# Kernel optimization log

Hardware: AMD Instinct MI355X
Metric: run time of the kernel (lower is better)

Reference implementation:

```python
import jax, jax.numpy as jnp
import numpy as np

B, LX, LY, D = 8, 2048, 2048, 256

def setup_inputs() -> dict:
    key = jax.random.key(0)
    k1, k2, k3, k4 = jax.random.split(key, 4)
    x = jax.random.normal(k1, (B, LX, D), dtype=jnp.float32)
    y = jax.random.normal(k2, (B, LY, D), dtype=jnp.float32)
    y_mask = jax.random.randint(k3, (B, LY), 0, 2).astype(jnp.bool_)
    W = jax.random.normal(k4, (D, D), dtype=jnp.float32) * (1.0 / np.sqrt(D))
    b = jnp.zeros((D,), dtype=jnp.float32)
    return {"x": x, "y": y, "y_mask": y_mask, "W": W, "b": b}

def reference(x, y, y_mask, W, b):
    # shared linear + relu projection (torch Linear: x @ W.T + b)
    x_proj = jax.nn.relu(jnp.einsum('bld,ed->ble', x, W) + b)  # [B,LX,D]
    y_proj = jax.nn.relu(jnp.einsum('bld,ed->ble', y, W) + b)  # [B,LY,D]
    scores = jnp.einsum('bxd,byd->bxy', x_proj, y_proj)        # [B,LX,LY]
    scores = jnp.where(y_mask[:, None, :], -jnp.inf, scores)
    alpha = jax.nn.softmax(scores, axis=-1)                    # [B,LX,LY]
    return jnp.einsum('bxy,byd->bxd', alpha, y)                # [B,LX,D]
```

## Files before the change

### kernel.cpp

```cpp
#include <hip/hip_runtime.h>

typedef __attribute__((ext_vector_type(8))) short short8;
typedef _Float16 half8 __attribute__((ext_vector_type(8)));
typedef __attribute__((ext_vector_type(4))) float f32x4;
typedef __attribute__((ext_vector_type(4))) unsigned int uint4v;
typedef __attribute__((ext_vector_type(2))) unsigned int uint2v;

#define B_   8
#define LX_  2048
#define LY_  2048
#define D_   256
#define NROW (B_ * LX_)
#define NQ   4

__device__ __forceinline__ unsigned short f2bf(float f) {
  unsigned u = __builtin_bit_cast(unsigned, f);
  u += 0x7FFF + ((u >> 16) & 1);
  return (unsigned short)(u >> 16);
}
__device__ __forceinline__ float bf2f(unsigned short h) {
  unsigned u = ((unsigned)h) << 16;
  return __builtin_bit_cast(float, u);
}

__global__ __launch_bounds__(256) void prep_kernel(
    const float* __restrict__ W, unsigned short* __restrict__ Whi,
    unsigned short* __restrict__ Wlo,
    const int* __restrict__ MASK, int* __restrict__ CIDX,
    int* __restrict__ CPOS, int* __restrict__ Lc) {
  int t = threadIdx.x;
  if (blockIdx.x >= 8) {
    int base = (blockIdx.x - 8) * 2048 + t * 8;
    f32x4 f0 = *(const f32x4*)(W + base);
    f32x4 f1 = *(const f32x4*)(W + base + 4);
    float v[8] = {f0[0], f0[1], f0[2], f0[3], f1[0], f1[1], f1[2], f1[3]};
    unsigned short h[8], l[8];
    for (int j = 0; j < 8; ++j) {
      h[j] = f2bf(v[j]);
      l[j] = f2bf(v[j] - bf2f(h[j]));
    }
    uint4v vh = {(unsigned)h[0] | ((unsigned)h[1] << 16), (unsigned)h[2] | ((unsigned)h[3] << 16),
                 (unsigned)h[4] | ((unsigned)h[5] << 16), (unsigned)h[6] | ((unsigned)h[7] << 16)};
    uint4v vl = {(unsigned)l[0] | ((unsigned)l[1] << 16), (unsigned)l[2] | ((unsigned)l[3] << 16),
                 (unsigned)l[4] | ((unsigned)l[5] << 16), (unsigned)l[6] | ((unsigned)l[7] << 16)};
    *(uint4v*)(Whi + base) = vh;
    *(uint4v*)(Wlo + base) = vl;
    return;
  }
  __shared__ int s[256];
  int b = blockIdx.x;
  int f[8];
  int cnt = 0;
  for (int k = 0; k < 8; ++k) {
    f[k] = (MASK[b * 2048 + t * 8 + k] == 0) ? 1 : 0;
    cnt += f[k];
  }
  s[t] = cnt;
  __syncthreads();
  for (int off = 1; off < 256; off <<= 1) {
    int v = (t >= off) ? s[t - off] : 0;
    __syncthreads();
    s[t] += v;
    __syncthreads();
  }
  if (t == 255) Lc[b] = s[255];
  int off = s[t] - cnt;
  for (int k = 0; k < 8; ++k) {
    int j = t * 8 + k;
    if (f[k]) {
      CIDX[b * 2048 + off] = j;
      CPOS[b * 2048 + j] = b * 2048 + off;
      ++off;
    } else {
      CPOS[b * 2048 + j] = -1;
    }
  }
}

__global__ __launch_bounds__(256, 2) void projgather_kernel(
    const float* __restrict__ X, const float* __restrict__ Y,
    const float* __restrict__ bias,
    const unsigned short* __restrict__ Whi, const unsigned short* __restrict__ Wlo,
    const int* __restrict__ CPOS, const int* __restrict__ CIDX,
    const int* __restrict__ Lc,
    _Float16* __restrict__ XP, _Float16* __restrict__ YPc,
    _Float16* __restrict__ YTc) {
  __shared__ __align__(16) unsigned char smem[51200];
  int t = threadIdx.x;

  if (blockIdx.x >= 512) {
    _Float16 (*tile)[72] = (_Float16(*)[72])smem;
    int id = blockIdx.x - 512;
    int db = id & 3, nb = (id >> 2) & 31, b = id >> 7;
    int lc = Lc[b];
    int end = (lc + 31) & ~31;
    if (nb * 64 >= end) return;
    int nl = t >> 2, ds = t & 3;
    int j = nb * 64 + nl;
    int idx = (j < lc) ? CIDX[b * 2048 + j] : 0;
    const float* src = Y + (size_t)(b * LY_ + idx) * D_ + db * 64 + ds * 16;
    for (int i = 0; i < 4; ++i) {
      f32x4 f = *(const f32x4*)(src + i * 4);
      for (int k = 0; k < 4; ++k) tile[ds * 16 + i * 4 + k][nl] = (_Float16)f[k];
    }
    __syncthreads();
    int dl = t >> 2, nsub = t & 3;
    uint4v v0 = *(const uint4v*)&tile[dl][nsub * 16];
    uint4v v1 = *(const uint4v*)&tile[dl][nsub * 16 + 8];
    _Float16* dst = YTc + (size_t)(b * D_ + db * 64 + dl) * LY_ + nb * 64 + nsub * 16;
    *(uint4v*)(dst) = v0;
    *(uint4v*)(dst + 8) = v1;
    return;
  }

  unsigned short (*Ah)[40] = (unsigned short(*)[40])(smem);
  unsigned short (*Al)[40] = (unsigned short(*)[40])(smem + 5120);
  unsigned short (*Bh)[40] = (unsigned short(*)[40])(smem + 10240);
  unsigned short (*Bl)[40] = (unsigned short(*)[40])(smem + 30720);

  int lane = t & 63, wave = t >> 6;
  int q = lane >> 4, n15 = lane & 15;

  bool isX = blockIdx.x < 256;
  const float* src = isX ? X : Y;
  int m0 = (isX ? blockIdx.x : (blockIdx.x - 256)) * 64;

  f32x4 acc[4][4];
  for (int mt = 0; mt < 4; ++mt)
    for (int nt = 0; nt < 4; ++nt) acc[mt][nt] = (f32x4){0.f, 0.f, 0.f, 0.f};

  int arow = t >> 2, aseg = t & 3;
  int erow = t >> 2, ec = t & 3;

  f32x4 pa[2];
  uint4v pbh[4], pbl[4];
#define PROJ_PF(kc)                                                            \
  {                                                                            \
    for (int i = 0; i < 2; ++i)                                                \
      pa[i] = *(const f32x4*)(src + (size_t)(m0 + arow) * D_ + (kc) * 32 +     \
                              (aseg + i * 4) * 4);                             \
    for (int p = 0; p < 4; ++p) {                                              \
      int e = p * 64 + erow;                                                   \
      pbh[p] = *(const uint4v*)(Whi + (size_t)e * D_ + (kc) * 32 + ec * 8);    \
      pbl[p] = *(const uint4v*)(Wlo + (size_t)e * D_ + (kc) * 32 + ec * 8);    \
    }                                                                          \
  }

  PROJ_PF(0);

  for (int kc = 0; kc < 8; ++kc) {
    __syncthreads();
    for (int i = 0; i < 2; ++i) {
      int seg = aseg + i * 4;
      f32x4 f = pa[i];
      unsigned short h[4], l[4];
      for (int j = 0; j < 4; ++j) {
        h[j] = f2bf(f[j]);
        l[j] = f2bf(f[j] - bf2f(h[j]));
      }
      uint2v vh = {(unsigned)h[0] | ((unsigned)h[1] << 16),
                   (unsigned)h[2] | ((unsigned)h[3] << 16)};
      uint2v vl = {(unsigned)l[0] | ((unsigned)l[1] << 16),
                   (unsigned)l[2] | ((unsigned)l[3] << 16)};
      *(uint2v*)&Ah[arow][seg * 4] = vh;
      *(uint2v*)&Al[arow][seg * 4] = vl;
    }
    for (int p = 0; p < 4; ++p) {
      int e = p * 64 + erow;
      *(uint4v*)&Bh[e][ec * 8] = pbh[p];
      *(uint4v*)&Bl[e][ec * 8] = pbl[p];
    }
    if (kc < 7) PROJ_PF(kc + 1);
    __syncthreads();

    short8 afh[4], afl[4], bfh[4], bfl[4];
    for (int mt = 0; mt < 4; ++mt) {
      afh[mt] = *(const short8*)&Ah[mt * 16 + n15][q * 8];
      afl[mt] = *(const short8*)&Al[mt * 16 + n15][q * 8];
    }
    for (int nt = 0; nt < 4; ++nt) {
      bfh[nt] = *(const short8*)&Bh[wave * 64 + nt * 16 + n15][q * 8];
      bfl[nt] = *(const short8*)&Bl[wave * 64 + nt * 16 + n15][q * 8];
    }
    for (int mt = 0; mt < 4; ++mt)
      for (int nt = 0; nt < 4; ++nt) {
        acc[mt][nt] = __builtin_amdgcn_mfma_f32_16x16x32_bf16(afh[mt], bfh[nt], acc[mt][nt], 0, 0, 0);
        acc[mt][nt] = __builtin_amdgcn_mfma_f32_16x16x32_bf16(afl[mt], bfh[nt], acc[mt][nt], 0, 0, 0);
        acc[mt][nt] = __builtin_amdgcn_mfma_f32_16x16x32_bf16(afh[mt], bfl[nt], acc[mt][nt], 0, 0, 0);
      }
  }
#undef PROJ_PF

  int drow[16];
  for (int mt = 0; mt < 4; ++mt)
    for (int r = 0; r < 4; ++r) {
      int row = m0 + mt * 16 + q * 4 + r;
      drow[mt * 4 + r] = isX ? row : CPOS[row];
    }
  _Float16* dst = isX ? XP : YPc;
  for (int nt = 0; nt < 4; ++nt) {
    int e = wave * 64 + nt * 16 + n15;
    float bv = bias[e];
    for (int mt = 0; mt < 4; ++mt)
      for (int r = 0; r < 4; ++r) {
        int dr = drow[mt * 4 + r];
        if (dr >= 0) {
          float v = acc[mt][nt][r] + bv;
          v = v > 0.f ? v : 0.f;
          dst[(size_t)dr * D_ + e] = (_Float16)v;
        }
      }
  }
}

__global__ __launch_bounds__(256, 2) void flash_kernel(
    const _Float16* __restrict__ XP, const _Float16* __restrict__ YPc,
    const _Float16* __restrict__ YTc, const int* __restrict__ Lc,
    _Float16* __restrict__ PO, float* __restrict__ Pm, float* __restrict__ Pl) {
  __shared__ _Float16 yp_t[32][264];
  __shared__ _Float16 yT_t[256][40];
  __shared__ _Float16 pbuf[4][16][40];

  int t = threadIdx.x;
  int lane = t & 63, wave = t >> 6;
  int q = lane >> 4, n15 = lane & 15;
  int qtr = blockIdx.x & 3;
  int xb = (blockIdx.x >> 2) & 31;
  int b = blockIdx.x >> 7;
  int row0 = xb * 64 + wave * 16;

  int lc = Lc[b];
  int T = (lc + 31) >> 5;
  int tstart = (T * qtr) >> 2;
  int tend   = (T * (qtr + 1)) >> 2;

  half8 a[8];
  const _Float16* xrow = XP + (size_t)(b * LX_ + row0 + n15) * D_ + q * 8;
  for (int kk = 0; kk < 8; ++kk) a[kk] = *(const half8*)(xrow + kk * 32);

  half8 lones;
  for (int j = 0; j < 8; ++j) lones[j] = (n15 == 0) ? (_Float16)1 : (_Float16)0;

  float m_r[4];
  for (int r = 0; r < 4; ++r) m_r[r] = -1e30f;
  f32x4 lacc = {0.f, 0.f, 0.f, 0.f};
  f32x4 oacc[16];
  for (int dt = 0; dt < 16; ++dt) oacc[dt] = (f32x4){0.f, 0.f, 0.f, 0.f};

  const _Float16* ypb = YPc + (size_t)b * LY_ * D_;
  const _Float16* yTb = YTc + (size_t)b * D_ * LY_;

  uint4v pr[8];
#define PREFETCH(tt)                                                          \
  {                                                                           \
    int y0p = (tt) * 32;                                                      \
    for (int i = 0; i < 4; ++i) {                                             \
      int c = t + i * 256;                                                    \
      pr[i] = *(const uint4v*)(ypb + (size_t)(y0p + (c >> 5)) * D_ + (c & 31) * 8); \
    }                                                                         \
    for (int i = 0; i < 4; ++i) {                                             \
      int c = t + i * 256;                                                    \
      pr[4 + i] = *(const uint4v*)(yTb + (size_t)(c >> 2) * LY_ + y0p + (c & 3) * 8); \
    }                                                                         \
  }

  if (tstart < tend) PREFETCH(tstart);

  for (int tt = tstart; tt < tend; ++tt) {
    int y0 = tt * 32;
    __syncthreads();
    for (int i = 0; i < 4; ++i) {
      int c = t + i * 256;
      *(uint4v*)&yp_t[c >> 5][(c & 31) * 8] = pr[i];
    }
    for (int i = 0; i < 4; ++i) {
      int c = t + i * 256;
      *(uint4v*)&yT_t[c >> 2][(c & 3) * 8] = pr[4 + i];
    }
    if (tt + 1 < tend) PREFETCH(tt + 1);
    __syncthreads();

    f32x4 S0 = {0.f, 0.f, 0.f, 0.f}, S1 = {0.f, 0.f, 0.f, 0.f};
    for (int kk = 0; kk < 8; ++kk) {
      half8 b0 = *(const half8*)&yp_t[n15][kk * 32 + q * 8];
      S0 = __builtin_amdgcn_mfma_f32_16x16x32_f16(a[kk], b0, S0, 0, 0, 0);
    }
    for (int kk = 0; kk < 8; ++kk) {
      half8 b1 = *(const half8*)&yp_t[16 + n15][kk * 32 + q * 8];
      S1 = __builtin_amdgcn_mfma_f32_16x16x32_f16(a[kk], b1, S1, 0, 0, 0);
    }
    bool mk0 = (y0 + n15) >= lc;
    bool mk1 = (y0 + 16 + n15) >= lc;

    float al[4];
    _Float16 ph0[4], ph1[4];
    bool need = false;
    for (int r = 0; r < 4; ++r) {
      float s0 = mk0 ? -1e30f : S0[r];
      float s1 = mk1 ? -1e30f : S1[r];
      float tm = fmaxf(s0, s1);
      tm = fmaxf(tm, __shfl_xor(tm, 1));
      tm = fmaxf(tm, __shfl_xor(tm, 2));
      tm = fmaxf(tm, __shfl_xor(tm, 4));
      tm = fmaxf(tm, __shfl_xor(tm, 8));
      float mn = fmaxf(m_r[r], tm);
      al[r] = __expf(m_r[r] - mn);
      m_r[r] = mn;
      ph0[r] = (_Float16)__expf(s0 - mn);
      ph1[r] = (_Float16)__expf(s1 - mn);
      need = need || (al[r] != 1.0f);
    }
    if (__ballot(need)) {
      for (int dt = 0; dt < 16; ++dt)
        for (int r = 0; r < 4; ++r) oacc[dt][r] *= al[r];
      for (int r = 0; r < 4; ++r) lacc[r] *= al[r];
    }
    for (int r = 0; r < 4; ++r) {
      pbuf[wave][q * 4 + r][n15] = ph0[r];
      pbuf[wave][q * 4 + r][16 + n15] = ph1[r];
    }
    half8 pa = *(const half8*)&pbuf[wave][n15][q * 8];
    lacc = __builtin_amdgcn_mfma_f32_16x16x32_f16(pa, lones, lacc, 0, 0, 0);
    for (int dt = 0; dt < 16; ++dt) {
      half8 bb = *(const half8*)&yT_t[dt * 16 + n15][q * 8];
      oacc[dt] = __builtin_amdgcn_mfma_f32_16x16x32_f16(pa, bb, oacc[dt], 0, 0, 0);
    }
  }
#undef PREFETCH

  size_t prow = (size_t)(qtr * B_ + b) * LX_ + row0;
  _Float16* po = PO + prow * D_;
  for (int dt = 0; dt < 16; ++dt)
    for (int r = 0; r < 4; ++r)
      po[(size_t)(q * 4 + r) * D_ + dt * 16 + n15] = (_Float16)oacc[dt][r];
  if (n15 == 0) {
    for (int r = 0; r < 4; ++r) {
      Pm[prow + q * 4 + r] = m_r[r];
      Pl[prow + q * 4 + r] = lacc[r];
    }
  }
}

__global__ __launch_bounds__(256) void merge_kernel(
    const _Float16* __restrict__ PO, const float* __restrict__ Pm,
    const float* __restrict__ Pl, float* __restrict__ OUT) {
  int c = blockIdx.x * 256 + threadIdx.x;
  int row = c >> 5, seg = c & 31;
  float m = -1e30f;
  float mh[NQ], lh[NQ];
  for (int h = 0; h < NQ; ++h) {
    mh[h] = Pm[(size_t)h * NROW + row];
    lh[h] = Pl[(size_t)h * NROW + row];
    m = fmaxf(m, mh[h]);
  }
  float l = 0.f;
  float wh[NQ];
  for (int h = 0; h < NQ; ++h) {
    wh[h] = __expf(mh[h] - m);
    l += lh[h] * wh[h];
  }
  float inv = 1.0f / l;
  float o[8];
  for (int j = 0; j < 8; ++j) o[j] = 0.f;
  for (int h = 0; h < NQ; ++h) {
    half8 a = *(const half8*)(PO + ((size_t)h * NROW + row) * D_ + seg * 8);
    float w = wh[h];
    for (int j = 0; j < 8; ++j) o[j] += (float)a[j] * w;
  }
  float* op = OUT + (size_t)row * D_ + seg * 8;
  f32x4 o0 = {o[0] * inv, o[1] * inv, o[2] * inv, o[3] * inv};
  f32x4 o1 = {o[4] * inv, o[5] * inv, o[6] * inv, o[7] * inv};
  *(f32x4*)op = o0;
  *(f32x4*)(op + 4) = o1;
}

extern "C" void kernel_launch(void* const* d_in, const int* in_sizes, int n_in,
                              void* d_out, int out_size, void* d_ws, size_t ws_size,
                              hipStream_t stream) {
  const float* x     = (const float*)d_in[0];
  const float* y     = (const float*)d_in[1];
  const int*   ymask = (const int*)  d_in[2];
  const float* W     = (const float*)d_in[3];
  const float* bias  = (const float*)d_in[4];
  float* out = (float*)d_out;

  char* ws = (char*)d_ws;
  size_t o = 0;
  unsigned short* Whi = (unsigned short*)(ws + o); o += 131072;
  unsigned short* Wlo = (unsigned short*)(ws + o); o += 131072;
  _Float16* XP  = (_Float16*)(ws + o); o += 8388608;
  _Float16* YPc = (_Float16*)(ws + o); o += 8388608;
  _Float16* YTc = (_Float16*)(ws + o); o += 8388608;
  _Float16* PO  = (_Float16*)(ws + o); o += (size_t)NQ * NROW * D_ * 2;
  float* Pm   = (float*)(ws + o); o += (size_t)NQ * NROW * 4;
  float* Pl   = (float*)(ws + o); o += (size_t)NQ * NROW * 4;
  int*   CIDX = (int*)  (ws + o); o += 65536;
  int*   CPOS = (int*)  (ws + o); o += 65536;
  int*   Lc   = (int*)  (ws + o);

  prep_kernel<<<40, 256, 0, stream>>>(W, Whi, Wlo, ymask, CIDX, CPOS, Lc);
  projgather_kernel<<<1536, 256, 0, stream>>>(x, y, bias, Whi, Wlo, CPOS, CIDX, Lc,
                                              XP, YPc, YTc);
  flash_kernel<<<1024, 256, 0, stream>>>(XP, YPc, YTc, Lc, PO, Pm, Pl);
  merge_kernel<<<2048, 256, 0, stream>>>(PO, Pm, Pl, out);
}
```

Before: 165.5 us.

## Project only unmasked Y rows and halve flash split-KV partitions

The Y projection now gathers rows through the compacted index list and skips blocks past the unmasked count, so masked rows are never projected. The scattered CPOS writes are replaced by staging the tile in shared memory and writing whole rows with coalesced vector stores. The flash kernel splits the key range into two partitions instead of four, which halves the grid and the partial-output traffic and simplifies the merge. The risk is lower occupancy and less parallelism in the flash kernel, which now has 512 blocks.

```diff
diff --git a/kernel.cpp b/kernel.cpp
--- a/kernel.cpp
+++ b/kernel.cpp
@@ -11,7 +11,6 @@
 #define LY_  2048
 #define D_   256
 #define NROW (B_ * LX_)
-#define NQ   4
 
 __device__ __forceinline__ unsigned short f2bf(float f) {
   unsigned u = __builtin_bit_cast(unsigned, f);
@@ -26,8 +25,7 @@
 __global__ __launch_bounds__(256) void prep_kernel(
     const float* __restrict__ W, unsigned short* __restrict__ Whi,
     unsigned short* __restrict__ Wlo,
-    const int* __restrict__ MASK, int* __restrict__ CIDX,
-    int* __restrict__ CPOS, int* __restrict__ Lc) {
+    const int* __restrict__ MASK, int* __restrict__ CIDX, int* __restrict__ Lc) {
   int t = threadIdx.x;
   if (blockIdx.x >= 8) {
     int base = (blockIdx.x - 8) * 2048 + t * 8;
@@ -67,13 +65,7 @@
   int off = s[t] - cnt;
   for (int k = 0; k < 8; ++k) {
     int j = t * 8 + k;
-    if (f[k]) {
-      CIDX[b * 2048 + off] = j;
-      CPOS[b * 2048 + j] = b * 2048 + off;
-      ++off;
-    } else {
-      CPOS[b * 2048 + j] = -1;
-    }
+    if (f[k]) CIDX[b * 2048 + (off++)] = j;
   }
 }
 
@@ -81,8 +73,7 @@
     const float* __restrict__ X, const float* __restrict__ Y,
     const float* __restrict__ bias,
     const unsigned short* __restrict__ Whi, const unsigned short* __restrict__ Wlo,
-    const int* __restrict__ CPOS, const int* __restrict__ CIDX,
-    const int* __restrict__ Lc,
+    const int* __restrict__ CIDX, const int* __restrict__ Lc,
     _Float16* __restrict__ XP, _Float16* __restrict__ YPc,
     _Float16* __restrict__ YTc) {
   __shared__ __align__(16) unsigned char smem[51200];
@@ -120,25 +111,37 @@
 
   int lane = t & 63, wave = t >> 6;
   int q = lane >> 4, n15 = lane & 15;
+  int arow = t >> 2, aseg = t & 3;
+  int erow = t >> 2, ec = t & 3;
 
   bool isX = blockIdx.x < 256;
-  const float* src = isX ? X : Y;
-  int m0 = (isX ? blockIdx.x : (blockIdx.x - 256)) * 64;
+  int m0 = 0, b = 0, slot0 = 0, lcb = 0;
+  const float* arow_ptr;
+  if (isX) {
+    m0 = blockIdx.x * 64;
+    arow_ptr = X + (size_t)(m0 + arow) * D_;
+  } else {
+    int id = blockIdx.x - 256;
+    b = id >> 5;
+    int rb = id & 31;
+    lcb = Lc[b];
+    slot0 = rb * 64;
+    if (slot0 >= lcb) return;
+    int sl = slot0 + arow;
+    int grow = (sl < lcb) ? CIDX[b * 2048 + sl] : 0;
+    arow_ptr = Y + (size_t)(b * 2048 + grow) * D_;
+  }
 
   f32x4 acc[4][4];
   for (int mt = 0; mt < 4; ++mt)
     for (int nt = 0; nt < 4; ++nt) acc[mt][nt] = (f32x4){0.f, 0.f, 0.f, 0.f};
-
-  int arow = t >> 2, aseg = t & 3;
-  int erow = t >> 2, ec = t & 3;
 
   f32x4 pa[2];
   uint4v pbh[4], pbl[4];
 #define PROJ_PF(kc)                                                            \
   {                                                                            \
     for (int i = 0; i < 2; ++i)                                                \
-      pa[i] = *(const f32x4*)(src + (size_t)(m0 + arow) * D_ + (kc) * 32 +     \
-                              (aseg + i * 4) * 4);                             \
+      pa[i] = *(const f32x4*)(arow_ptr + (kc) * 32 + (aseg + i * 4) * 4);      \
     for (int p = 0; p < 4; ++p) {                                              \
       int e = p * 64 + erow;                                                   \
       pbh[p] = *(const uint4v*)(Whi + (size_t)e * D_ + (kc) * 32 + ec * 8);    \
@@ -191,25 +194,28 @@
   }
 #undef PROJ_PF
 
-  int drow[16];
-  for (int mt = 0; mt < 4; ++mt)
-    for (int r = 0; r < 4; ++r) {
-      int row = m0 + mt * 16 + q * 4 + r;
-      drow[mt * 4 + r] = isX ? row : CPOS[row];
-    }
-  _Float16* dst = isX ? XP : YPc;
+  __syncthreads();
+  _Float16 (*epi)[264] = (_Float16(*)[264])smem;
   for (int nt = 0; nt < 4; ++nt) {
     int e = wave * 64 + nt * 16 + n15;
     float bv = bias[e];
     for (int mt = 0; mt < 4; ++mt)
       for (int r = 0; r < 4; ++r) {
-        int dr = drow[mt * 4 + r];
-        if (dr >= 0) {
-          float v = acc[mt][nt][r] + bv;
-          v = v > 0.f ? v : 0.f;
-          dst[(size_t)dr * D_ + e] = (_Float16)v;
-        }
+        float v = acc[mt][nt][r] + bv;
+        v = v > 0.f ? v : 0.f;
+        epi[mt * 16 + q * 4 + r][e] = (_Float16)v;
       }
+  }
+  __syncthreads();
+  int row = t >> 2, seg = t & 3;
+  bool valid = isX || (slot0 + row < lcb);
+  if (valid) {
+    _Float16* drp = isX ? (XP + (size_t)(m0 + row) * D_)
+                        : (YPc + (size_t)(b * 2048 + slot0 + row) * D_);
+    for (int k = 0; k < 8; ++k) {
+      uint4v v = *(const uint4v*)&epi[row][seg * 64 + k * 8];
+      *(uint4v*)(drp + seg * 64 + k * 8) = v;
+    }
   }
 }
 
@@ -224,15 +230,16 @@
   int t = threadIdx.x;
   int lane = t & 63, wave = t >> 6;
   int q = lane >> 4, n15 = lane & 15;
-  int qtr = blockIdx.x & 3;
-  int xb = (blockIdx.x >> 2) & 31;
-  int b = blockIdx.x >> 7;
+  int half = blockIdx.x & 1;
+  int xb = (blockIdx.x >> 1) & 31;
+  int b = blockIdx.x >> 6;
   int row0 = xb * 64 + wave * 16;
 
   int lc = Lc[b];
-  int T = (lc + 31) >> 5;
-  int tstart = (T * qtr) >> 2;
-  int tend   = (T * (qtr + 1)) >> 2;
+  int T  = (lc + 31) >> 5;
+  int T0 = (T + 1) >> 1;
+  int tstart = half ? T0 : 0;
+  int tend   = half ? T  : T0;
 
   half8 a[8];
   const _Float16* xrow = XP + (size_t)(b * LX_ + row0 + n15) * D_ + q * 8;
@@ -328,7 +335,7 @@
   }
 #undef PREFETCH
 
-  size_t prow = (size_t)(qtr * B_ + b) * LX_ + row0;
+  size_t prow = (size_t)(half * B_ + b) * LX_ + row0;
   _Float16* po = PO + prow * D_;
   for (int dt = 0; dt < 16; ++dt)
     for (int r = 0; r < 4; ++r)
@@ -346,32 +353,21 @@
     const float* __restrict__ Pl, float* __restrict__ OUT) {
   int c = blockIdx.x * 256 + threadIdx.x;
   int row = c >> 5, seg = c & 31;
-  float m = -1e30f;
-  float mh[NQ], lh[NQ];
-  for (int h = 0; h < NQ; ++h) {
-    mh[h] = Pm[(size_t)h * NROW + row];
-    lh[h] = Pl[(size_t)h * NROW + row];
-    m = fmaxf(m, mh[h]);
-  }
-  float l = 0.f;
-  float wh[NQ];
-  for (int h = 0; h < NQ; ++h) {
-    wh[h] = __expf(mh[h] - m);
-    l += lh[h] * wh[h];
-  }
-  float inv = 1.0f / l;
-  float o[8];
-  for (int j = 0; j < 8; ++j) o[j] = 0.f;
-  for (int h = 0; h < NQ; ++h) {
-    half8 a = *(const half8*)(PO + ((size_t)h * NROW + row) * D_ + seg * 8);
-    float w = wh[h];
-    for (int j = 0; j < 8; ++j) o[j] += (float)a[j] * w;
-  }
-  float* op = OUT + (size_t)row * D_ + seg * 8;
-  f32x4 o0 = {o[0] * inv, o[1] * inv, o[2] * inv, o[3] * inv};
-  f32x4 o1 = {o[4] * inv, o[5] * inv, o[6] * inv, o[7] * inv};
-  *(f32x4*)op = o0;
-  *(f32x4*)(op + 4) = o1;
+  float m0 = Pm[row], m1 = Pm[NROW + row];
+  float l0 = Pl[row], l1 = Pl[NROW + row];
+  float m = fmaxf(m0, m1);
+  float w0 = __expf(m0 - m), w1 = __expf(m1 - m);
+  float inv = 1.0f / (l0 * w0 + l1 * w1);
+  const _Float16* p0 = PO + (size_t)row * D_ + seg * 8;
+  const _Float16* p1 = p0 + (size_t)NROW * D_;
+  half8 a = *(const half8*)p0;
+  half8 bsec = *(const half8*)p1;
+  float* o = OUT + (size_t)row * D_ + seg * 8;
+  f32x4 o0, o1;
+  for (int j = 0; j < 4; ++j) o0[j] = ((float)a[j] * w0 + (float)bsec[j] * w1) * inv;
+  for (int j = 0; j < 4; ++j) o1[j] = ((float)a[4 + j] * w0 + (float)bsec[4 + j] * w1) * inv;
+  *(f32x4*)o = o0;
+  *(f32x4*)(o + 4) = o1;
 }
 
 extern "C" void kernel_launch(void* const* d_in, const int* in_sizes, int n_in,
@@ -391,16 +387,15 @@
   _Float16* XP  = (_Float16*)(ws + o); o += 8388608;
   _Float16* YPc = (_Float16*)(ws + o); o += 8388608;
   _Float16* YTc = (_Float16*)(ws + o); o += 8388608;
-  _Float16* PO  = (_Float16*)(ws + o); o += (size_t)NQ * NROW * D_ * 2;
-  float* Pm   = (float*)(ws + o); o += (size_t)NQ * NROW * 4;
-  float* Pl   = (float*)(ws + o); o += (size_t)NQ * NROW * 4;
+  _Float16* PO  = (_Float16*)(ws + o); o += 16777216;
+  float* Pm   = (float*)(ws + o); o += 131072;
+  float* Pl   = (float*)(ws + o); o += 131072;
   int*   CIDX = (int*)  (ws + o); o += 65536;
-  int*   CPOS = (int*)  (ws + o); o += 65536;
   int*   Lc   = (int*)  (ws + o);
 
-  prep_kernel<<<40, 256, 0, stream>>>(W, Whi, Wlo, ymask, CIDX, CPOS, Lc);
-  projgather_kernel<<<1536, 256, 0, stream>>>(x, y, bias, Whi, Wlo, CPOS, CIDX, Lc,
+  prep_kernel<<<40, 256, 0, stream>>>(W, Whi, Wlo, ymask, CIDX, Lc);
+  projgather_kernel<<<1536, 256, 0, stream>>>(x, y, bias, Whi, Wlo, CIDX, Lc,
                                               XP, YPc, YTc);
-  flash_kernel<<<1024, 256, 0, stream>>>(XP, YPc, YTc, Lc, PO, Pm, Pl);
+  flash_kernel<<<512, 256, 0, stream>>>(XP, YPc, YTc, Lc, PO, Pm, Pl);
   merge_kernel<<<2048, 256, 0, stream>>>(PO, Pm, Pl, out);
 }
```

Result: faster. 155.0 us (-6.3%).
